# Kernel tuning notes

Measured on AMD Instinct MI355X. Metric: run time of the kernel, lower is better.

## Reference

```python
import jax, jax.numpy as jnp
import numpy as np

N_FRAMES = 64
N_ATOMS = 512
SEG_LEN = 1


def get_segments(n_atoms: int, length: int) -> np.ndarray:
    """All ordered pairs of chain segments (i,i+L),(j,j+L) that share no atoms (j-i>L)."""
    starts = np.arange(n_atoms - length)
    i, j = np.meshgrid(starts, starts, indexing='ij')
    mask = (j - i) > length
    i, j = i[mask], j[mask]
    return np.stack([i, i + length, j, j + length], axis=1).astype(np.int32)


def setup_inputs() -> dict:
    key = jax.random.key(0)
    xyz = jax.random.normal(key, (N_FRAMES, N_ATOMS, 3), dtype=jnp.float32)
    segments = jnp.asarray(get_segments(N_ATOMS, SEG_LEN))  # (P, 4) int32
    return {"xyz": xyz, "segments": segments}


def _unit(v):
    return v / jnp.linalg.norm(v, axis=-1, keepdims=True)


def reference(xyz, segments):
    # xyz: (F, N, 3); segments: (P, 4) = [i, i+L, j, j+L]
    p1 = xyz[:, segments[:, 0]]  # (F, P, 3)
    p2 = xyz[:, segments[:, 1]]
    p3 = xyz[:, segments[:, 2]]
    p4 = xyz[:, segments[:, 3]]

    r12 = p2 - p1
    r13 = p3 - p1
    r14 = p4 - p1
    r23 = p3 - p2
    r24 = p4 - p2
    r34 = p4 - p3

    # unit normals of the four faces of the tetrahedron spanned by the segment pair
    n1 = _unit(jnp.cross(r13, r14))
    n2 = _unit(jnp.cross(r14, r24))
    n3 = _unit(jnp.cross(r24, r23))
    n4 = _unit(jnp.cross(r23, r13))

    def asin_dot(a, b):
        return jnp.arcsin(jnp.clip(jnp.sum(a * b, axis=-1), -1.0, 1.0))

    # Gauss linking integral (Klenin & Langowski) per segment pair
    theta = asin_dot(n1, n2) + asin_dot(n2, n3) + asin_dot(n3, n4) + asin_dot(n4, n1)
    sign = jnp.sign(jnp.sum(jnp.cross(r34, r12) * r13, axis=-1))
    wr = theta * sign / (2.0 * jnp.pi)  # (F, P)
    return wr
```

## Files before the change

### kernel.cpp

```cpp
#include <hip/hip_runtime.h>
#include <math.h>

#define NFRAMES 64
#define NATOMS  512
#define NSEG    129795
#define NROWS   509
#define BLOCK   128
#define RUN     4

typedef float v2 __attribute__((ext_vector_type(2)));

__device__ __forceinline__ v2 v2s(float x) { v2 r; r.x = x; r.y = x; return r; }
__device__ __forceinline__ v2 v2mk(float a, float b) { v2 r; r.x = a; r.y = b; return r; }
__device__ __forceinline__ v2 vfma(v2 a, v2 b, v2 c) { return __builtin_elementwise_fma(a, b, c); }
__device__ __forceinline__ v2 vabs(v2 x) { v2 r; r.x = fabsf(x.x); r.y = fabsf(x.y); return r; }
__device__ __forceinline__ v2 vmin1(v2 a) { v2 r; r.x = fminf(a.x, 1.0f); r.y = fminf(a.y, 1.0f); return r; }
__device__ __forceinline__ v2 vsqrt_raw(v2 x) {
    v2 r; r.x = __builtin_amdgcn_sqrtf(x.x); r.y = __builtin_amdgcn_sqrtf(x.y); return r;
}
__device__ __forceinline__ v2 vrsq_raw(v2 x) {
    v2 r; r.x = __builtin_amdgcn_rsqf(x.x); r.y = __builtin_amdgcn_rsqf(x.y); return r;
}
__device__ __forceinline__ v2 vcopysign(v2 m, v2 s) {
    v2 r; r.x = copysignf(m.x, s.x); r.y = copysignf(m.y, s.y); return r;
}

__device__ __forceinline__ v2 vasin(v2 x) {
    v2 ax = vmin1(vabs(x));
    v2 p  = vfma(ax, v2s(-0.156582f), v2s(1.565019f));
    v2 r  = v2s(1.57079632679f) - vsqrt_raw(v2s(1.0f) - ax) * p;
    return vcopysign(r, x);
}

struct v23 { v2 x, y, z; };

__device__ __forceinline__ v23 vcross(v23 a, v23 b) {
    return v23{ vfma(a.y, b.z, -(a.z * b.y)),
                vfma(a.z, b.x, -(a.x * b.z)),
                vfma(a.x, b.y, -(a.y * b.x)) };
}
__device__ __forceinline__ v2 vdot(v23 a, v23 b) {
    return vfma(a.x, b.x, vfma(a.y, b.y, a.z * b.z));
}

__device__ __forceinline__ int b2(int a) { return 3 * a + (a >> 2); }
#define LDS_V2 1680

__global__ __launch_bounds__(BLOCK) void writhe_kernel(
    const float* __restrict__ xyz,
    float*       __restrict__ out)
{
    __shared__ v2 sp[LDS_V2];

    const int b  = blockIdx.x;
    const int f0 = blockIdx.y * 2;
    const float* fxa = xyz + (size_t)f0 * (NATOMS * 3);
    const float* fxb = fxa + NATOMS * 3;
    for (int a = threadIdx.x; a < NATOMS; a += BLOCK) {
        const float* g0 = fxa + 3 * a;
        const float* g1 = fxb + 3 * a;
        const int s = b2(a);
        sp[s + 0] = v2mk(g0[0], g1[0]);
        sp[s + 1] = v2mk(g0[1], g1[1]);
        sp[s + 2] = v2mk(g0[2], g1[2]);
    }
    if (threadIdx.x < 3) {
        const int s = b2(NATOMS + threadIdx.x);
        sp[s + 0] = v2s(0.f); sp[s + 1] = v2s(0.f); sp[s + 2] = v2s(0.f);
    }
    __syncthreads();

    int rowA, rowB, lenB;
    if (b < 253)       { rowA = b + 2; rowB = 508 - b; lenB = b + 1; }
    else if (b == 253) { rowA = 1;     rowB = 0;       lenB = 0;     }
    else if (b == 254) { rowA = 0;     rowB = 0;       lenB = 0;     }
    else               { rowA = 255;   rowB = 0;       lenB = 0;     }
    const int lenA = NROWS - rowA;
    const int na   = (lenA + 3) >> 2;

    const int t    = threadIdx.x;
    const bool inA = (t < na);
    const int row  = inA ? rowA : rowB;
    const int len  = inA ? lenA : lenB;
    const int k0   = (inA ? t : (t - na)) << 2;
    if (k0 >= len) return;

    const int j0 = row + 2 + k0;

    v2 Ax[RUN + 1], Ay[RUN + 1], Az[RUN + 1];
    #pragma unroll
    for (int m = 0; m <= RUN; ++m) {
        const int s = b2(j0 + m);
        Ax[m] = sp[s]; Ay[m] = sp[s + 1]; Az[m] = sp[s + 2];
    }
    const int sP1 = b2(row), sP2 = b2(row + 1);
    const v2 P1x = sp[sP1], P1y = sp[sP1 + 1], P1z = sp[sP1 + 2];
    const v2 P2x = sp[sP2], P2y = sp[sP2 + 1], P2z = sp[sP2 + 2];

    v23 u[RUN + 1], vv[RUN + 1], w34[RUN];
    #pragma unroll
    for (int m = 0; m <= RUN; ++m) {
        u[m]  = v23{Ax[m] - P1x, Ay[m] - P1y, Az[m] - P1z};
        vv[m] = v23{Ax[m] - P2x, Ay[m] - P2y, Az[m] - P2z};
    }
    #pragma unroll
    for (int m = 0; m < RUN; ++m)
        w34[m] = v23{Ax[m+1] - Ax[m], Ay[m+1] - Ay[m], Az[m+1] - Az[m]};
    const v23 s12{P2x - P1x, P2y - P1y, P2z - P1z};

    v23 h  = vcross(u[0], vv[0]);
    v2 in4 = vrsq_raw(vdot(h, h));

    const int off = NROWS * row - (row * (row - 1)) / 2;
    const size_t base0 = (size_t)f0 * NSEG + off + k0;
    const int rem = len - k0;

    #pragma unroll
    for (int k = 0; k < RUN; ++k) {
        v23 c1 = vcross(u[k],      u[k + 1]);
        v23 c2 = vcross(u[k + 1],  vv[k + 1]);
        v23 c3 = vcross(vv[k + 1], vv[k]);

        v2 in1 = vrsq_raw(vdot(c1, c1));
        v2 in2 = vrsq_raw(vdot(c2, c2));
        v2 in3 = vrsq_raw(vdot(c3, c3));

        v2 d12 = vdot(c1, c2) * (in1 * in2);
        v2 d23 = vdot(c2, c3) * (in2 * in3);
        v2 e34 = vdot(c3, h)  * (in3 * in4);
        v2 e41 = vdot(h, c1)  * (in4 * in1);

        v2 theta = (vasin(d12) + vasin(d23)) - (vasin(e34) + vasin(e41));

        v2 sv = vdot(vcross(w34[k], s12), u[k]);
        v2 wr = theta * vcopysign(v2s(0.15915494309189535f), sv);
        wr.x = (sv.x == 0.0f) ? 0.0f : wr.x;
        wr.y = (sv.y == 0.0f) ? 0.0f : wr.y;

        if (k < rem) {
            out[base0 + k]        = wr.x;
            out[base0 + k + NSEG] = wr.y;
        }
        h = c2; in4 = in2;
    }
}

extern "C" void kernel_launch(void* const* d_in, const int* in_sizes, int n_in,
                              void* d_out, int out_size, void* d_ws, size_t ws_size,
                              hipStream_t stream) {
    const float* xyz = (const float*)d_in[0];
    float*       out = (float*)d_out;

    dim3 grid(256, NFRAMES / 2);
    writhe_kernel<<<grid, BLOCK, 0, stream>>>(xyz, out);
}
```

Measured before the change: 84.06 us.

## Use 256-thread blocks with 2 pairs per thread and simpler row pairing

Each thread now handles 2 consecutive segment pairs instead of 4, and blocks grow to 256 threads. Rows are paired as b and 508-b across 255 blocks, replacing the previous special-case mapping. Difference vectors are recomputed inside the loop rather than kept in arrays, and launch bounds request 6 blocks per CU to cut register pressure. The aim is more parallelism and occupancy, at the cost of loading more shared memory per output and losing some reuse across the run.

```diff
diff --git a/kernel.cpp b/kernel.cpp
--- a/kernel.cpp
+++ b/kernel.cpp
@@ -5,8 +5,9 @@
 #define NATOMS  512
 #define NSEG    129795
 #define NROWS   509
-#define BLOCK   128
-#define RUN     4
+#define NBLK    255
+#define BLOCK   256
+#define RUN     2
 
 typedef float v2 __attribute__((ext_vector_type(2)));
 
@@ -46,7 +47,7 @@
 __device__ __forceinline__ int b2(int a) { return 3 * a + (a >> 2); }
 #define LDS_V2 1680
 
-__global__ __launch_bounds__(BLOCK) void writhe_kernel(
+__global__ __launch_bounds__(BLOCK, 6) void writhe_kernel(
     const float* __restrict__ xyz,
     float*       __restrict__ out)
 {
@@ -70,19 +71,17 @@
     }
     __syncthreads();
 
-    int rowA, rowB, lenB;
-    if (b < 253)       { rowA = b + 2; rowB = 508 - b; lenB = b + 1; }
-    else if (b == 253) { rowA = 1;     rowB = 0;       lenB = 0;     }
-    else if (b == 254) { rowA = 0;     rowB = 0;       lenB = 0;     }
-    else               { rowA = 255;   rowB = 0;       lenB = 0;     }
+    const int rowA = b;
+    const int rowB = 508 - b;
     const int lenA = NROWS - rowA;
-    const int na   = (lenA + 3) >> 2;
+    const int lenB = (rowB == rowA) ? 0 : NROWS - rowB;
+    const int na   = (lenA + 1) >> 1;
 
     const int t    = threadIdx.x;
     const bool inA = (t < na);
     const int row  = inA ? rowA : rowB;
     const int len  = inA ? lenA : lenB;
-    const int k0   = (inA ? t : (t - na)) << 2;
+    const int k0   = (inA ? t : (t - na)) << 1;
     if (k0 >= len) return;
 
     const int j0 = row + 2 + k0;
@@ -96,19 +95,11 @@
     const int sP1 = b2(row), sP2 = b2(row + 1);
     const v2 P1x = sp[sP1], P1y = sp[sP1 + 1], P1z = sp[sP1 + 2];
     const v2 P2x = sp[sP2], P2y = sp[sP2 + 1], P2z = sp[sP2 + 2];
-
-    v23 u[RUN + 1], vv[RUN + 1], w34[RUN];
-    #pragma unroll
-    for (int m = 0; m <= RUN; ++m) {
-        u[m]  = v23{Ax[m] - P1x, Ay[m] - P1y, Az[m] - P1z};
-        vv[m] = v23{Ax[m] - P2x, Ay[m] - P2y, Az[m] - P2z};
-    }
-    #pragma unroll
-    for (int m = 0; m < RUN; ++m)
-        w34[m] = v23{Ax[m+1] - Ax[m], Ay[m+1] - Ay[m], Az[m+1] - Az[m]};
     const v23 s12{P2x - P1x, P2y - P1y, P2z - P1z};
 
-    v23 h  = vcross(u[0], vv[0]);
+    v23 u0{Ax[0] - P1x, Ay[0] - P1y, Az[0] - P1z};
+    v23 vv0{Ax[0] - P2x, Ay[0] - P2y, Az[0] - P2z};
+    v23 h  = vcross(u0, vv0);
     v2 in4 = vrsq_raw(vdot(h, h));
 
     const int off = NROWS * row - (row * (row - 1)) / 2;
@@ -117,9 +108,15 @@
 
     #pragma unroll
     for (int k = 0; k < RUN; ++k) {
-        v23 c1 = vcross(u[k],      u[k + 1]);
-        v23 c2 = vcross(u[k + 1],  vv[k + 1]);
-        v23 c3 = vcross(vv[k + 1], vv[k]);
+        v23 uk {Ax[k]     - P1x, Ay[k]     - P1y, Az[k]     - P1z};
+        v23 uk1{Ax[k + 1] - P1x, Ay[k + 1] - P1y, Az[k + 1] - P1z};
+        v23 vk {Ax[k]     - P2x, Ay[k]     - P2y, Az[k]     - P2z};
+        v23 vk1{Ax[k + 1] - P2x, Ay[k + 1] - P2y, Az[k + 1] - P2z};
+        v23 w34{Ax[k + 1] - Ax[k], Ay[k + 1] - Ay[k], Az[k + 1] - Az[k]};
+
+        v23 c1 = vcross(uk,  uk1);
+        v23 c2 = vcross(uk1, vk1);
+        v23 c3 = vcross(vk1, vk);
 
         v2 in1 = vrsq_raw(vdot(c1, c1));
         v2 in2 = vrsq_raw(vdot(c2, c2));
@@ -132,7 +129,7 @@
 
         v2 theta = (vasin(d12) + vasin(d23)) - (vasin(e34) + vasin(e41));
 
-        v2 sv = vdot(vcross(w34[k], s12), u[k]);
+        v2 sv = vdot(vcross(w34, s12), uk);
         v2 wr = theta * vcopysign(v2s(0.15915494309189535f), sv);
         wr.x = (sv.x == 0.0f) ? 0.0f : wr.x;
         wr.y = (sv.y == 0.0f) ? 0.0f : wr.y;
@@ -151,6 +148,6 @@
     const float* xyz = (const float*)d_in[0];
     float*       out = (float*)d_out;
 
-    dim3 grid(256, NFRAMES / 2);
+    dim3 grid(NBLK, NFRAMES / 2);
     writhe_kernel<<<grid, BLOCK, 0, stream>>>(xyz, out);
 }
```

Result: slower. 88.81 us (+5.6%).
